# Kernel optimization log

Hardware: AMD Instinct MI355X
Metric: run time of the kernel (lower is better)

Reference implementation:

```python
import jax, jax.numpy as jnp
import numpy as np

N_NODES = 50000
N_EDGES = 800000
D = 128
N_REL = 4
N_GRAPHS = 128
N_CLASSES = 16


def rgcn_layer(x, W_rel, W_root, b, src, dst, edge_type):
    # Per-relation transform of all nodes: [N, R, D]
    xt = jnp.einsum('nd,rdf->nrf', x, W_rel)
    msg = xt[src, edge_type]  # [E, D] gather message per edge
    # mean aggregation per (dst, relation) pair (PyG RGCNConv aggr='mean')
    seg = dst * N_REL + edge_type
    cnt = jax.ops.segment_sum(jnp.ones((src.shape[0],), x.dtype), seg,
                              num_segments=N_NODES * N_REL)
    norm = 1.0 / jnp.maximum(cnt[seg], 1.0)
    agg = jax.ops.segment_sum(msg * norm[:, None], dst, num_segments=N_NODES)
    return agg + x @ W_root + b


def setup_inputs() -> dict:
    key = jax.random.key(0)
    ks = jax.random.split(key, 12)
    s = 1.0 / np.sqrt(D)
    inp = {
        'x': jax.random.normal(ks[0], (N_NODES, D), jnp.float32),
        'edge_index': jax.random.randint(ks[1], (2, N_EDGES), 0, N_NODES, jnp.int64),
        'edge_type': jax.random.randint(ks[2], (N_EDGES,), 0, N_REL, jnp.int64),
        'batch': jnp.sort(jax.random.randint(ks[3], (N_NODES,), 0, N_GRAPHS, jnp.int64)),
        'W_rel1': jax.random.normal(ks[4], (N_REL, D, D), jnp.float32) * s,
        'W_root1': jax.random.normal(ks[5], (D, D), jnp.float32) * s,
        'b1': jnp.zeros((D,), jnp.float32),
        'W_rel2': jax.random.normal(ks[6], (N_REL, D, D), jnp.float32) * s,
        'W_root2': jax.random.normal(ks[7], (D, D), jnp.float32) * s,
        'b2': jnp.zeros((D,), jnp.float32),
        'W_cls': jax.random.normal(ks[8], (D, N_CLASSES), jnp.float32) * s,
        'b_cls': jnp.zeros((N_CLASSES,), jnp.float32),
    }
    return inp


def reference(x, edge_index, edge_type, batch, W_rel1, W_root1, b1,
              W_rel2, W_root2, b2, W_cls, b_cls):
    src, dst = edge_index[0], edge_index[1]
    h = jax.nn.relu(rgcn_layer(x, W_rel1, W_root1, b1, src, dst, edge_type))
    h = jax.nn.relu(rgcn_layer(h, W_rel2, W_root2, b2, src, dst, edge_type))
    # global mean pool over graphs (dropout is identity: training=False)
    gsum = jax.ops.segment_sum(h, batch, num_segments=N_GRAPHS)
    gcnt = jax.ops.segment_sum(jnp.ones((h.shape[0],), h.dtype), batch,
                               num_segments=N_GRAPHS)
    g = gsum / jnp.maximum(gcnt, 1.0)[:, None]
    return g @ W_cls + b_cls
```

## Files before the change

kernel.cpp:

```cpp
#include <hip/hip_runtime.h>

#define D_DIM 128
#define N_REL 4
#define CAP 32

typedef __attribute__((ext_vector_type(8))) short bf16x8;
typedef __attribute__((ext_vector_type(4))) float f32x4;

static inline int cdiv(int a, int b) { return (a + b - 1) / b; }

__device__ inline ushort f2bf(float f) {
    union { float f; unsigned u; } v;
    v.f = f;
    unsigned r = v.u + 0x7FFFu + ((v.u >> 16) & 1u);
    return (ushort)(r >> 16);
}

__device__ inline float bf2f(ushort u) {
    union { unsigned u; float f; } v;
    v.u = (unsigned)u << 16;
    return v.f;
}

__device__ inline float uif(unsigned u) {
    union { unsigned u; float f; } v;
    v.u = u;
    return v.f;
}

#define CNT_B 391
#define CAST_B 6250
#define PACK_B 80

__global__ __launch_bounds__(256) void prep_kernel(
    const float* __restrict__ x, ushort* __restrict__ Xb,
    const int* __restrict__ src, const int* __restrict__ dst,
    const int* __restrict__ et, unsigned* __restrict__ icnt,
    int* __restrict__ esorted,
    const float* __restrict__ Wrel1, const float* __restrict__ Wroot1,
    const float* __restrict__ Wrel2, const float* __restrict__ Wroot2,
    ushort* __restrict__ Wpk1, ushort* __restrict__ Wpk2,
    int n4, int nEdges) {
    int b = blockIdx.x;
    if (b < CNT_B) {
        int e = (b * 256 + threadIdx.x) * 8;
        if (e >= nEdges) return;
        if (e + 8 <= nEdges) {
            int4 sA = *(const int4*)(src + e);
            int4 sB = *(const int4*)(src + e + 4);
            int4 dA = *(const int4*)(dst + e);
            int4 dB = *(const int4*)(dst + e + 4);
            int4 tA = *(const int4*)(et + e);
            int4 tB = *(const int4*)(et + e + 4);
            unsigned o0 = atomicAdd(&icnt[dA.x], 1u << (8 * tA.x));
            unsigned o1 = atomicAdd(&icnt[dA.y], 1u << (8 * tA.y));
            unsigned o2 = atomicAdd(&icnt[dA.z], 1u << (8 * tA.z));
            unsigned o3 = atomicAdd(&icnt[dA.w], 1u << (8 * tA.w));
            unsigned o4 = atomicAdd(&icnt[dB.x], 1u << (8 * tB.x));
            unsigned o5 = atomicAdd(&icnt[dB.y], 1u << (8 * tB.y));
            unsigned o6 = atomicAdd(&icnt[dB.z], 1u << (8 * tB.z));
            unsigned o7 = atomicAdd(&icnt[dB.w], 1u << (8 * tB.w));
            int r0 = (int)(((o0 >> (8 * tA.x)) & 0xFFu) - 0xAAu);
            int r1 = (int)(((o1 >> (8 * tA.y)) & 0xFFu) - 0xAAu);
            int r2 = (int)(((o2 >> (8 * tA.z)) & 0xFFu) - 0xAAu);
            int r3 = (int)(((o3 >> (8 * tA.w)) & 0xFFu) - 0xAAu);
            int r4 = (int)(((o4 >> (8 * tB.x)) & 0xFFu) - 0xAAu);
            int r5 = (int)(((o5 >> (8 * tB.y)) & 0xFFu) - 0xAAu);
            int r6 = (int)(((o6 >> (8 * tB.z)) & 0xFFu) - 0xAAu);
            int r7 = (int)(((o7 >> (8 * tB.w)) & 0xFFu) - 0xAAu);
            esorted[((size_t)(dA.x * N_REL + tA.x) << 5) + r0] = sA.x;
            esorted[((size_t)(dA.y * N_REL + tA.y) << 5) + r1] = sA.y;
            esorted[((size_t)(dA.z * N_REL + tA.z) << 5) + r2] = sA.z;
            esorted[((size_t)(dA.w * N_REL + tA.w) << 5) + r3] = sA.w;
            esorted[((size_t)(dB.x * N_REL + tB.x) << 5) + r4] = sB.x;
            esorted[((size_t)(dB.y * N_REL + tB.y) << 5) + r5] = sB.y;
            esorted[((size_t)(dB.z * N_REL + tB.z) << 5) + r6] = sB.z;
            esorted[((size_t)(dB.w * N_REL + tB.w) << 5) + r7] = sB.w;
        } else {
            for (int j = 0; e + j < nEdges; ++j) {
                int dd = dst[e + j], tt = et[e + j];
                unsigned o = atomicAdd(&icnt[dd], 1u << (8 * tt));
                int r = (int)(((o >> (8 * tt)) & 0xFFu) - 0xAAu);
                esorted[((size_t)(dd * N_REL + tt) << 5) + r] = src[e + j];
            }
        }
    } else if (b < CNT_B + CAST_B) {
        int i = (b - CNT_B) * 256 + threadIdx.x;
        if (i < n4) {
            float4 v = ((const float4*)x)[i];
            ushort4 o;
            o.x = f2bf(v.x); o.y = f2bf(v.y); o.z = f2bf(v.z); o.w = f2bf(v.w);
            ((ushort4*)Xb)[i] = o;
        }
    } else {
        int pb = b - (CNT_B + CAST_B);
        int layer = pb / 40;
        int rem = pb % 40;
        int mat = rem >> 3;
        int blk = rem & 7;
        const float* Wrel = layer ? Wrel2 : Wrel1;
        const float* Wroot = layer ? Wroot2 : Wroot1;
        ushort* out = layer ? Wpk2 : Wpk1;
        const float* W = (mat < N_REL) ? (Wrel + (size_t)mat * D_DIM * D_DIM) : Wroot;
        int t = blk * 256 + threadIdx.x;
        int lane = t & 63;
        int tile = t >> 6;
        int kt = tile >> 3;
        int nt = tile & 7;
        int n = nt * 16 + (lane & 15);
        int kb = kt * 32 + (lane >> 4) * 8;
        ushort* o = out + (((size_t)mat * 32 + tile) * 64 + lane) * 8;
        ushort4 lo, hi;
        lo.x = f2bf(W[(kb + 0) * D_DIM + n]);
        lo.y = f2bf(W[(kb + 1) * D_DIM + n]);
        lo.z = f2bf(W[(kb + 2) * D_DIM + n]);
        lo.w = f2bf(W[(kb + 3) * D_DIM + n]);
        hi.x = f2bf(W[(kb + 4) * D_DIM + n]);
        hi.y = f2bf(W[(kb + 5) * D_DIM + n]);
        hi.z = f2bf(W[(kb + 6) * D_DIM + n]);
        hi.w = f2bf(W[(kb + 7) * D_DIM + n]);
        *(ushort4*)(o) = lo;
        *(ushort4*)(o + 4) = hi;
    }
}

__global__ __launch_bounds__(256) void layer_kernel(
    const ushort* __restrict__ Xb, const unsigned* __restrict__ icnt,
    const int* __restrict__ esorted, const ushort* __restrict__ Wpk,
    const float* __restrict__ bias, ushort* __restrict__ outb, int n_nodes) {
    __shared__ ushort Ms[16][520];
    __shared__ int ids[16][33];
    __shared__ int sids[16][33];
    const int tid = threadIdx.x;
    const int wave = tid >> 6;
    const int lane = tid & 63;
    const int ql = tid & 15;
    const int qd = tid >> 4;
    const int m = lane & 15;
    const int q = lane >> 4;
    const int r0 = blockIdx.x * 16;

    auto acc8 = [](float* a, uint4 u) {
        a[0] += uif(u.x << 16); a[1] += uif(u.x & 0xFFFF0000u);
        a[2] += uif(u.y << 16); a[3] += uif(u.y & 0xFFFF0000u);
        a[4] += uif(u.z << 16); a[5] += uif(u.z & 0xFFFF0000u);
        a[6] += uif(u.w << 16); a[7] += uif(u.w & 0xFFFF0000u);
    };

    for (int p = 0; p < 4; ++p) {
        const int segl = p * 16 + qd;
        const int row = segl >> 2;
        const int rel = segl & 3;
        const int node = r0 + row;
        int deg = 0;
        if (node < n_nodes) {
            unsigned w = icnt[node];
            deg = (int)(((w >> (rel * 8)) & 0xFFu) - 0xAAu);
        }
        uint4* mrow = (uint4*)&Ms[row][rel * 128 + ql * 8];
        const ushort* xb = Xb + ql * 8;
        const int* eb = esorted + ((size_t)((node << 2) + rel) << 5);
        if (deg == 0) {
            *mrow = make_uint4(0u, 0u, 0u, 0u);
        } else if (deg == 1) {
            *mrow = *(const uint4*)(xb + (size_t)eb[0] * D_DIM);
        } else {
            for (int j = ql; j < deg; j += 16) ids[qd][j] = eb[j];
            __threadfence_block();
#pragma unroll
            for (int base = 0; base < 2; ++base) {
                int j = base * 16 + ql;
                if (j < deg) {
                    int v = ids[qd][j];
                    int rank = 0;
                    for (int k = 0; k < deg; ++k) {
                        int w = ids[qd][k];
                        rank += (w < v || (w == v && k < j)) ? 1 : 0;
                    }
                    sids[qd][rank] = v;
                }
            }
            __threadfence_block();
            float a[8], b[8];
#pragma unroll
            for (int j = 0; j < 8; ++j) { a[j] = 0.f; b[j] = 0.f; }
            int e = 0;
            for (; e + 4 <= deg; e += 4) {
                int s0 = sids[qd][e];
                int s1 = sids[qd][e + 1];
                int s2 = sids[qd][e + 2];
                int s3 = sids[qd][e + 3];
                uint4 u0 = *(const uint4*)(xb + (size_t)s0 * D_DIM);
                uint4 u1 = *(const uint4*)(xb + (size_t)s1 * D_DIM);
                uint4 u2 = *(const uint4*)(xb + (size_t)s2 * D_DIM);
                uint4 u3 = *(const uint4*)(xb + (size_t)s3 * D_DIM);
                acc8(a, u0); acc8(b, u1); acc8(a, u2); acc8(b, u3);
            }
            if (e + 2 <= deg) {
                int s0 = sids[qd][e];
                int s1 = sids[qd][e + 1];
                uint4 u0 = *(const uint4*)(xb + (size_t)s0 * D_DIM);
                uint4 u1 = *(const uint4*)(xb + (size_t)s1 * D_DIM);
                acc8(a, u0); acc8(b, u1);
                e += 2;
            }
            if (e < deg) {
                uint4 u0 = *(const uint4*)(xb + (size_t)sids[qd][e] * D_DIM);
                acc8(a, u0);
            }
            float sc = 1.0f / (float)deg;
            uint4 o;
            o.x = (unsigned)f2bf((a[0] + b[0]) * sc) | ((unsigned)f2bf((a[1] + b[1]) * sc) << 16);
            o.y = (unsigned)f2bf((a[2] + b[2]) * sc) | ((unsigned)f2bf((a[3] + b[3]) * sc) << 16);
            o.z = (unsigned)f2bf((a[4] + b[4]) * sc) | ((unsigned)f2bf((a[5] + b[5]) * sc) << 16);
            o.w = (unsigned)f2bf((a[6] + b[6]) * sc) | ((unsigned)f2bf((a[7] + b[7]) * sc) << 16);
            *mrow = o;
        }
    }
    __syncthreads();

    f32x4 acc0 = (f32x4){0.f, 0.f, 0.f, 0.f};
    f32x4 acc1 = (f32x4){0.f, 0.f, 0.f, 0.f};
#pragma unroll
    for (int ph = 0; ph < N_REL; ++ph) {
        const ushort* Bp = Wpk + (size_t)ph * (32 * 64 * 8);
#pragma unroll
        for (int kt = 0; kt < 4; ++kt) {
            bf16x8 a = *(const bf16x8*)&Ms[m][ph * 128 + kt * 32 + q * 8];
            bf16x8 b0 = *(const bf16x8*)(Bp + ((size_t)(kt * 8 + wave * 2) * 64 + lane) * 8);
            bf16x8 b1 = *(const bf16x8*)(Bp + ((size_t)(kt * 8 + wave * 2 + 1) * 64 + lane) * 8);
            acc0 = __builtin_amdgcn_mfma_f32_16x16x32_bf16(a, b0, acc0, 0, 0, 0);
            acc1 = __builtin_amdgcn_mfma_f32_16x16x32_bf16(a, b1, acc1, 0, 0, 0);
        }
    }
    {
        const int n0 = min(r0 + m, n_nodes - 1);
        const ushort* aX = Xb + (size_t)n0 * D_DIM + q * 8;
        const ushort* Bp = Wpk + (size_t)N_REL * (32 * 64 * 8);
#pragma unroll
        for (int kt = 0; kt < 4; ++kt) {
            bf16x8 a = *(const bf16x8*)(aX + kt * 32);
            bf16x8 b0 = *(const bf16x8*)(Bp + ((size_t)(kt * 8 + wave * 2) * 64 + lane) * 8);
            bf16x8 b1 = *(const bf16x8*)(Bp + ((size_t)(kt * 8 + wave * 2 + 1) * 64 + lane) * 8);
            acc0 = __builtin_amdgcn_mfma_f32_16x16x32_bf16(a, b0, acc0, 0, 0, 0);
            acc1 = __builtin_amdgcn_mfma_f32_16x16x32_bf16(a, b1, acc1, 0, 0, 0);
        }
    }

#pragma unroll
    for (int j = 0; j < 2; ++j) {
        const f32x4 av = j ? acc1 : acc0;
        int col = (wave * 2 + j) * 16 + m;
        float bv = bias[col];
#pragma unroll
        for (int r = 0; r < 4; ++r) {
            int row = r0 + q * 4 + r;
            if (row < n_nodes)
                outb[(size_t)row * D_DIM + col] = f2bf(fmaxf(av[r] + bv, 0.0f));
        }
    }
}

__global__ __launch_bounds__(1024) void poolcls_kernel(
    const ushort* __restrict__ hb, const int* __restrict__ batch,
    const float* __restrict__ Wcls, const float* __restrict__ bcls,
    float* __restrict__ out, int n_nodes) {
    __shared__ float part[64][D_DIM + 1];
    __shared__ float mean[D_DIM];
    __shared__ float cpart[16][17];
    int g = blockIdx.x;
    int tid = threadIdx.x;
    int par = tid >> 4;
    int dg = (tid & 15) * 8;
    auto lb = [&](int val) {
        int lo = 0, hi = n_nodes;
        while (lo < hi) {
            int mid = (lo + hi) >> 1;
            if (batch[mid] < val) lo = mid + 1; else hi = mid;
        }
        return lo;
    };
    int lo = lb(g), hi = lb(g + 1);
    float a[8];
#pragma unroll
    for (int j = 0; j < 8; ++j) a[j] = 0.f;
    for (int nn = lo + par; nn < hi; nn += 64) {
        uint4 u = *(const uint4*)(hb + (size_t)nn * D_DIM + dg);
        a[0] += uif(u.x << 16); a[1] += uif(u.x & 0xFFFF0000u);
        a[2] += uif(u.y << 16); a[3] += uif(u.y & 0xFFFF0000u);
        a[4] += uif(u.z << 16); a[5] += uif(u.z & 0xFFFF0000u);
        a[6] += uif(u.w << 16); a[7] += uif(u.w & 0xFFFF0000u);
    }
#pragma unroll
    for (int j = 0; j < 8; ++j) part[par][dg + j] = a[j];
    __syncthreads();
    if (tid < D_DIM) {
        float s = 0.f;
#pragma unroll
        for (int j = 0; j < 64; ++j) s += part[j][tid];
        mean[tid] = s / fmaxf((float)(hi - lo), 1.0f);
    }
    __syncthreads();
    if (tid < 256) {
        int c = tid & 15, kc = tid >> 4;
        float s = 0.f;
#pragma unroll
        for (int j = 0; j < 8; ++j)
            s = fmaf(mean[kc * 8 + j], Wcls[(kc * 8 + j) * 16 + c], s);
        cpart[kc][c] = s;
    }
    __syncthreads();
    if (tid < 16) {
        float s = bcls[tid];
#pragma unroll
        for (int k = 0; k < 16; ++k) s += cpart[k][tid];
        out[g * 16 + tid] = s;
    }
}

extern "C" void kernel_launch(void* const* d_in, const int* in_sizes, int n_in,
                              void* d_out, int out_size, void* d_ws, size_t ws_size,
                              hipStream_t stream) {
    const float* x      = (const float*)d_in[0];
    const int*   ei     = (const int*)d_in[1];
    const int*   etype  = (const int*)d_in[2];
    const int*   batch  = (const int*)d_in[3];
    const float* Wrel1  = (const float*)d_in[4];
    const float* Wroot1 = (const float*)d_in[5];
    const float* b1     = (const float*)d_in[6];
    const float* Wrel2  = (const float*)d_in[7];
    const float* Wroot2 = (const float*)d_in[8];
    const float* b2     = (const float*)d_in[9];
    const float* Wcls   = (const float*)d_in[10];
    const float* bcls   = (const float*)d_in[11];
    float* out = (float*)d_out;

    const int N = in_sizes[0] / D_DIM;
    const int E = in_sizes[1] / 2;
    const int* src = ei;
    const int* dst = ei + E;

    ushort* Xb   = (ushort*)d_ws;
    ushort* h1b  = Xb + (size_t)N * D_DIM;
    ushort* h2b  = h1b + (size_t)N * D_DIM;
    ushort* M    = h2b + (size_t)N * D_DIM;
    ushort* Wpk1 = M + (size_t)N * N_REL * D_DIM;
    ushort* Wpk2 = Wpk1 + 81920;
    unsigned* icnt = (unsigned*)(Wpk2 + 81920);
    int* esorted = (int*)(icnt + N);

    prep_kernel<<<CNT_B + CAST_B + PACK_B, 256, 0, stream>>>(
        x, Xb, src, dst, etype, icnt, esorted, Wrel1, Wroot1, Wrel2, Wroot2,
        Wpk1, Wpk2, N * D_DIM / 4, E);

    layer_kernel<<<cdiv(N, 16), 256, 0, stream>>>(
        Xb, icnt, esorted, Wpk1, b1, h1b, N);

    layer_kernel<<<cdiv(N, 16), 256, 0, stream>>>(
        h1b, icnt, esorted, Wpk2, b2, h2b, N);

    poolcls_kernel<<<128, 1024, 0, stream>>>(h2b, batch, Wcls, bcls, out, N);
}
```

Measured before the change: 270.0 us.

## Sort edge lists once in separate kernel, 16-bit ids, 32-row layer tiles

Moves the per-segment sort of source ids out of both layer kernels into a separate sort_kernel that runs once, so the two layers no longer repeat it. Edge source ids are stored as 16-bit values to halve index traffic, and each thread prefetches its id rows and counts up front. The layer kernel now handles 32 nodes per block with 512 threads, with each wave sharing one B fragment across two row tiles, and the gather loop is unrolled to 8 loads. Storing ids as ushort assumes node ids stay below 65536, which holds for 50000 nodes but not in general, and the extra kernel launch adds overhead.

```diff
diff --git a/kernel.cpp b/kernel.cpp
--- a/kernel.cpp
+++ b/kernel.cpp
@@ -36,7 +36,7 @@
     const float* __restrict__ x, ushort* __restrict__ Xb,
     const int* __restrict__ src, const int* __restrict__ dst,
     const int* __restrict__ et, unsigned* __restrict__ icnt,
-    int* __restrict__ esorted,
+    ushort* __restrict__ esorted,
     const float* __restrict__ Wrel1, const float* __restrict__ Wroot1,
     const float* __restrict__ Wrel2, const float* __restrict__ Wroot2,
     ushort* __restrict__ Wpk1, ushort* __restrict__ Wpk2,
@@ -68,20 +68,20 @@
             int r5 = (int)(((o5 >> (8 * tB.y)) & 0xFFu) - 0xAAu);
             int r6 = (int)(((o6 >> (8 * tB.z)) & 0xFFu) - 0xAAu);
             int r7 = (int)(((o7 >> (8 * tB.w)) & 0xFFu) - 0xAAu);
-            esorted[((size_t)(dA.x * N_REL + tA.x) << 5) + r0] = sA.x;
-            esorted[((size_t)(dA.y * N_REL + tA.y) << 5) + r1] = sA.y;
-            esorted[((size_t)(dA.z * N_REL + tA.z) << 5) + r2] = sA.z;
-            esorted[((size_t)(dA.w * N_REL + tA.w) << 5) + r3] = sA.w;
-            esorted[((size_t)(dB.x * N_REL + tB.x) << 5) + r4] = sB.x;
-            esorted[((size_t)(dB.y * N_REL + tB.y) << 5) + r5] = sB.y;
-            esorted[((size_t)(dB.z * N_REL + tB.z) << 5) + r6] = sB.z;
-            esorted[((size_t)(dB.w * N_REL + tB.w) << 5) + r7] = sB.w;
+            esorted[((size_t)(dA.x * N_REL + tA.x) << 5) + r0] = (ushort)sA.x;
+            esorted[((size_t)(dA.y * N_REL + tA.y) << 5) + r1] = (ushort)sA.y;
+            esorted[((size_t)(dA.z * N_REL + tA.z) << 5) + r2] = (ushort)sA.z;
+            esorted[((size_t)(dA.w * N_REL + tA.w) << 5) + r3] = (ushort)sA.w;
+            esorted[((size_t)(dB.x * N_REL + tB.x) << 5) + r4] = (ushort)sB.x;
+            esorted[((size_t)(dB.y * N_REL + tB.y) << 5) + r5] = (ushort)sB.y;
+            esorted[((size_t)(dB.z * N_REL + tB.z) << 5) + r6] = (ushort)sB.z;
+            esorted[((size_t)(dB.w * N_REL + tB.w) << 5) + r7] = (ushort)sB.w;
         } else {
             for (int j = 0; e + j < nEdges; ++j) {
                 int dd = dst[e + j], tt = et[e + j];
                 unsigned o = atomicAdd(&icnt[dd], 1u << (8 * tt));
                 int r = (int)(((o >> (8 * tt)) & 0xFFu) - 0xAAu);
-                esorted[((size_t)(dd * N_REL + tt) << 5) + r] = src[e + j];
+                esorted[((size_t)(dd * N_REL + tt) << 5) + r] = (ushort)src[e + j];
             }
         }
     } else if (b < CNT_B + CAST_B) {
@@ -124,13 +124,55 @@
     }
 }
 
-__global__ __launch_bounds__(256) void layer_kernel(
+__global__ __launch_bounds__(256) void sort_kernel(
+    const unsigned* __restrict__ icnt, ushort* __restrict__ esorted, int nseg) {
+    __shared__ int ids[16][34];
+    __shared__ int sids[16][34];
+    const int tid = threadIdx.x;
+    const int ql = tid & 15;
+    const int qd = tid >> 4;
+    const int seg = blockIdx.x * 16 + qd;
+    if (seg >= nseg) return;
+    unsigned w = icnt[seg >> 2];
+    int deg = (int)(((w >> ((seg & 3) * 8)) & 0xFFu) - 0xAAu);
+    if (deg < 2) return;
+    ushort* row = esorted + ((size_t)seg << 5);
+    unsigned u = ((const unsigned*)row)[ql];
+    ids[qd][2 * ql] = (int)(u & 0xFFFFu);
+    ids[qd][2 * ql + 1] = (int)(u >> 16);
+    __threadfence_block();
+#pragma unroll
+    for (int base = 0; base < 2; ++base) {
+        int j = base * 16 + ql;
+        if (j < deg) {
+            int v = ids[qd][j];
+            int rank = 0;
+            int k = 0;
+            for (; k + 4 <= deg; k += 4) {
+                int w0 = ids[qd][k], w1 = ids[qd][k + 1];
+                int w2 = ids[qd][k + 2], w3 = ids[qd][k + 3];
+                rank += (w0 < v || (w0 == v && k < j)) ? 1 : 0;
+                rank += (w1 < v || (w1 == v && k + 1 < j)) ? 1 : 0;
+                rank += (w2 < v || (w2 == v && k + 2 < j)) ? 1 : 0;
+                rank += (w3 < v || (w3 == v && k + 3 < j)) ? 1 : 0;
+            }
+            for (; k < deg; ++k) {
+                int wv = ids[qd][k];
+                rank += (wv < v || (wv == v && k < j)) ? 1 : 0;
+            }
+            sids[qd][rank] = v;
+        }
+    }
+    __threadfence_block();
+    for (int j = ql; j < deg; j += 16) row[j] = (ushort)sids[qd][j];
+}
+
+__global__ __launch_bounds__(512) void layer_kernel(
     const ushort* __restrict__ Xb, const unsigned* __restrict__ icnt,
-    const int* __restrict__ esorted, const ushort* __restrict__ Wpk,
+    const ushort* __restrict__ esorted, const ushort* __restrict__ Wpk,
     const float* __restrict__ bias, ushort* __restrict__ outb, int n_nodes) {
-    __shared__ ushort Ms[16][520];
-    __shared__ int ids[16][33];
-    __shared__ int sids[16][33];
+    __shared__ ushort Ms[32][520];
+    __shared__ int ids[32][34];
     const int tid = threadIdx.x;
     const int wave = tid >> 6;
     const int lane = tid & 63;
@@ -138,7 +180,20 @@
     const int qd = tid >> 4;
     const int m = lane & 15;
     const int q = lane >> 4;
-    const int r0 = blockIdx.x * 16;
+    const int r0 = blockIdx.x * 32;
+    const int rel = qd & 3;
+    const int rbase = qd >> 2;
+
+    unsigned id4[4], cnt4[4];
+#pragma unroll
+    for (int p = 0; p < 4; ++p) {
+        int node = r0 + p * 8 + rbase;
+        int vnode = min(node, n_nodes - 1);
+        cnt4[p] = icnt[vnode];
+        const ushort* eb = esorted + ((size_t)((vnode << 2) + rel) << 5);
+        id4[p] = ((const unsigned*)eb)[ql];
+        if (node >= n_nodes) cnt4[p] = 0xAAAAAAAAu;
+    }
 
     auto acc8 = [](float* a, uint4 u) {
         a[0] += uif(u.x << 16); a[1] += uif(u.x & 0xFFFF0000u);
@@ -148,74 +203,65 @@
     };
 
     for (int p = 0; p < 4; ++p) {
-        const int segl = p * 16 + qd;
-        const int row = segl >> 2;
-        const int rel = segl & 3;
-        const int node = r0 + row;
-        int deg = 0;
-        if (node < n_nodes) {
-            unsigned w = icnt[node];
-            deg = (int)(((w >> (rel * 8)) & 0xFFu) - 0xAAu);
-        }
+        const int row = p * 8 + rbase;
+        const int deg = (int)(((cnt4[p] >> (rel * 8)) & 0xFFu) - 0xAAu);
         uint4* mrow = (uint4*)&Ms[row][rel * 128 + ql * 8];
         const ushort* xb = Xb + ql * 8;
-        const int* eb = esorted + ((size_t)((node << 2) + rel) << 5);
-        if (deg == 0) {
+        if (deg <= 0) {
             *mrow = make_uint4(0u, 0u, 0u, 0u);
-        } else if (deg == 1) {
-            *mrow = *(const uint4*)(xb + (size_t)eb[0] * D_DIM);
-        } else {
-            for (int j = ql; j < deg; j += 16) ids[qd][j] = eb[j];
-            __threadfence_block();
-#pragma unroll
-            for (int base = 0; base < 2; ++base) {
-                int j = base * 16 + ql;
-                if (j < deg) {
-                    int v = ids[qd][j];
-                    int rank = 0;
-                    for (int k = 0; k < deg; ++k) {
-                        int w = ids[qd][k];
-                        rank += (w < v || (w == v && k < j)) ? 1 : 0;
-                    }
-                    sids[qd][rank] = v;
-                }
-            }
-            __threadfence_block();
-            float a[8], b[8];
-#pragma unroll
-            for (int j = 0; j < 8; ++j) { a[j] = 0.f; b[j] = 0.f; }
-            int e = 0;
-            for (; e + 4 <= deg; e += 4) {
-                int s0 = sids[qd][e];
-                int s1 = sids[qd][e + 1];
-                int s2 = sids[qd][e + 2];
-                int s3 = sids[qd][e + 3];
-                uint4 u0 = *(const uint4*)(xb + (size_t)s0 * D_DIM);
-                uint4 u1 = *(const uint4*)(xb + (size_t)s1 * D_DIM);
-                uint4 u2 = *(const uint4*)(xb + (size_t)s2 * D_DIM);
-                uint4 u3 = *(const uint4*)(xb + (size_t)s3 * D_DIM);
-                acc8(a, u0); acc8(b, u1); acc8(a, u2); acc8(b, u3);
-            }
-            if (e + 2 <= deg) {
-                int s0 = sids[qd][e];
-                int s1 = sids[qd][e + 1];
-                uint4 u0 = *(const uint4*)(xb + (size_t)s0 * D_DIM);
-                uint4 u1 = *(const uint4*)(xb + (size_t)s1 * D_DIM);
-                acc8(a, u0); acc8(b, u1);
-                e += 2;
-            }
-            if (e < deg) {
-                uint4 u0 = *(const uint4*)(xb + (size_t)sids[qd][e] * D_DIM);
-                acc8(a, u0);
-            }
-            float sc = 1.0f / (float)deg;
-            uint4 o;
-            o.x = (unsigned)f2bf((a[0] + b[0]) * sc) | ((unsigned)f2bf((a[1] + b[1]) * sc) << 16);
-            o.y = (unsigned)f2bf((a[2] + b[2]) * sc) | ((unsigned)f2bf((a[3] + b[3]) * sc) << 16);
-            o.z = (unsigned)f2bf((a[4] + b[4]) * sc) | ((unsigned)f2bf((a[5] + b[5]) * sc) << 16);
-            o.w = (unsigned)f2bf((a[6] + b[6]) * sc) | ((unsigned)f2bf((a[7] + b[7]) * sc) << 16);
-            *mrow = o;
-        }
+            continue;
+        }
+        ids[qd][2 * ql] = (int)(id4[p] & 0xFFFFu);
+        ids[qd][2 * ql + 1] = (int)(id4[p] >> 16);
+        __threadfence_block();
+        float a[8], b[8];
+#pragma unroll
+        for (int j = 0; j < 8; ++j) { a[j] = 0.f; b[j] = 0.f; }
+        int e = 0;
+        for (; e + 8 <= deg; e += 8) {
+            int s0 = ids[qd][e],     s1 = ids[qd][e + 1];
+            int s2 = ids[qd][e + 2], s3 = ids[qd][e + 3];
+            int s4 = ids[qd][e + 4], s5 = ids[qd][e + 5];
+            int s6 = ids[qd][e + 6], s7 = ids[qd][e + 7];
+            uint4 u0 = *(const uint4*)(xb + (size_t)s0 * D_DIM);
+            uint4 u1 = *(const uint4*)(xb + (size_t)s1 * D_DIM);
+            uint4 u2 = *(const uint4*)(xb + (size_t)s2 * D_DIM);
+            uint4 u3 = *(const uint4*)(xb + (size_t)s3 * D_DIM);
+            uint4 u4 = *(const uint4*)(xb + (size_t)s4 * D_DIM);
+            uint4 u5 = *(const uint4*)(xb + (size_t)s5 * D_DIM);
+            uint4 u6 = *(const uint4*)(xb + (size_t)s6 * D_DIM);
+            uint4 u7 = *(const uint4*)(xb + (size_t)s7 * D_DIM);
+            acc8(a, u0); acc8(b, u1); acc8(a, u2); acc8(b, u3);
+            acc8(a, u4); acc8(b, u5); acc8(a, u6); acc8(b, u7);
+        }
+        if (e + 4 <= deg) {
+            int s0 = ids[qd][e], s1 = ids[qd][e + 1];
+            int s2 = ids[qd][e + 2], s3 = ids[qd][e + 3];
+            uint4 u0 = *(const uint4*)(xb + (size_t)s0 * D_DIM);
+            uint4 u1 = *(const uint4*)(xb + (size_t)s1 * D_DIM);
+            uint4 u2 = *(const uint4*)(xb + (size_t)s2 * D_DIM);
+            uint4 u3 = *(const uint4*)(xb + (size_t)s3 * D_DIM);
+            acc8(a, u0); acc8(b, u1); acc8(a, u2); acc8(b, u3);
+            e += 4;
+        }
+        if (e + 2 <= deg) {
+            int s0 = ids[qd][e], s1 = ids[qd][e + 1];
+            uint4 u0 = *(const uint4*)(xb + (size_t)s0 * D_DIM);
+            uint4 u1 = *(const uint4*)(xb + (size_t)s1 * D_DIM);
+            acc8(a, u0); acc8(b, u1);
+            e += 2;
+        }
+        if (e < deg) {
+            uint4 u0 = *(const uint4*)(xb + (size_t)ids[qd][e] * D_DIM);
+            acc8(a, u0);
+        }
+        float sc = 1.0f / (float)deg;
+        uint4 o;
+        o.x = (unsigned)f2bf((a[0] + b[0]) * sc) | ((unsigned)f2bf((a[1] + b[1]) * sc) << 16);
+        o.y = (unsigned)f2bf((a[2] + b[2]) * sc) | ((unsigned)f2bf((a[3] + b[3]) * sc) << 16);
+        o.z = (unsigned)f2bf((a[4] + b[4]) * sc) | ((unsigned)f2bf((a[5] + b[5]) * sc) << 16);
+        o.w = (unsigned)f2bf((a[6] + b[6]) * sc) | ((unsigned)f2bf((a[7] + b[7]) * sc) << 16);
+        *mrow = o;
     }
     __syncthreads();
 
@@ -223,40 +269,42 @@
     f32x4 acc1 = (f32x4){0.f, 0.f, 0.f, 0.f};
 #pragma unroll
     for (int ph = 0; ph < N_REL; ++ph) {
-        const ushort* Bp = Wpk + (size_t)ph * (32 * 64 * 8);
 #pragma unroll
         for (int kt = 0; kt < 4; ++kt) {
-            bf16x8 a = *(const bf16x8*)&Ms[m][ph * 128 + kt * 32 + q * 8];
-            bf16x8 b0 = *(const bf16x8*)(Bp + ((size_t)(kt * 8 + wave * 2) * 64 + lane) * 8);
-            bf16x8 b1 = *(const bf16x8*)(Bp + ((size_t)(kt * 8 + wave * 2 + 1) * 64 + lane) * 8);
-            acc0 = __builtin_amdgcn_mfma_f32_16x16x32_bf16(a, b0, acc0, 0, 0, 0);
-            acc1 = __builtin_amdgcn_mfma_f32_16x16x32_bf16(a, b1, acc1, 0, 0, 0);
+            bf16x8 b = *(const bf16x8*)(Wpk + (((size_t)ph * 32 + kt * 8 + wave) * 64 + lane) * 8);
+            bf16x8 a0 = *(const bf16x8*)&Ms[m][ph * 128 + kt * 32 + q * 8];
+            bf16x8 a1 = *(const bf16x8*)&Ms[16 + m][ph * 128 + kt * 32 + q * 8];
+            acc0 = __builtin_amdgcn_mfma_f32_16x16x32_bf16(a0, b, acc0, 0, 0, 0);
+            acc1 = __builtin_amdgcn_mfma_f32_16x16x32_bf16(a1, b, acc1, 0, 0, 0);
         }
     }
     {
         const int n0 = min(r0 + m, n_nodes - 1);
-        const ushort* aX = Xb + (size_t)n0 * D_DIM + q * 8;
-        const ushort* Bp = Wpk + (size_t)N_REL * (32 * 64 * 8);
+        const int n1 = min(r0 + 16 + m, n_nodes - 1);
+        const ushort* aX0 = Xb + (size_t)n0 * D_DIM + q * 8;
+        const ushort* aX1 = Xb + (size_t)n1 * D_DIM + q * 8;
 #pragma unroll
         for (int kt = 0; kt < 4; ++kt) {
-            bf16x8 a = *(const bf16x8*)(aX + kt * 32);
-            bf16x8 b0 = *(const bf16x8*)(Bp + ((size_t)(kt * 8 + wave * 2) * 64 + lane) * 8);
-            bf16x8 b1 = *(const bf16x8*)(Bp + ((size_t)(kt * 8 + wave * 2 + 1) * 64 + lane) * 8);
-            acc0 = __builtin_amdgcn_mfma_f32_16x16x32_bf16(a, b0, acc0, 0, 0, 0);
-            acc1 = __builtin_amdgcn_mfma_f32_16x16x32_bf16(a, b1, acc1, 0, 0, 0);
-        }
-    }
-
-#pragma unroll
-    for (int j = 0; j < 2; ++j) {
-        const f32x4 av = j ? acc1 : acc0;
-        int col = (wave * 2 + j) * 16 + m;
+            bf16x8 b = *(const bf16x8*)(Wpk + (((size_t)N_REL * 32 + kt * 8 + wave) * 64 + lane) * 8);
+            bf16x8 a0 = *(const bf16x8*)(aX0 + kt * 32);
+            bf16x8 a1 = *(const bf16x8*)(aX1 + kt * 32);
+            acc0 = __builtin_amdgcn_mfma_f32_16x16x32_bf16(a0, b, acc0, 0, 0, 0);
+            acc1 = __builtin_amdgcn_mfma_f32_16x16x32_bf16(a1, b, acc1, 0, 0, 0);
+        }
+    }
+
+    {
+        int col = wave * 16 + m;
         float bv = bias[col];
 #pragma unroll
-        for (int r = 0; r < 4; ++r) {
-            int row = r0 + q * 4 + r;
-            if (row < n_nodes)
-                outb[(size_t)row * D_DIM + col] = f2bf(fmaxf(av[r] + bv, 0.0f));
+        for (int rt = 0; rt < 2; ++rt) {
+            const f32x4 av = rt ? acc1 : acc0;
+#pragma unroll
+            for (int r = 0; r < 4; ++r) {
+                int row = r0 + rt * 16 + q * 4 + r;
+                if (row < n_nodes)
+                    outb[(size_t)row * D_DIM + col] = f2bf(fmaxf(av[r] + bv, 0.0f));
+            }
         }
     }
 }
@@ -337,26 +385,28 @@
 
     const int N = in_sizes[0] / D_DIM;
     const int E = in_sizes[1] / 2;
+    const int NSEG = N * N_REL;
     const int* src = ei;
     const int* dst = ei + E;
 
     ushort* Xb   = (ushort*)d_ws;
     ushort* h1b  = Xb + (size_t)N * D_DIM;
     ushort* h2b  = h1b + (size_t)N * D_DIM;
-    ushort* M    = h2b + (size_t)N * D_DIM;
-    ushort* Wpk1 = M + (size_t)N * N_REL * D_DIM;
+    ushort* Wpk1 = h2b + (size_t)N * D_DIM;
     ushort* Wpk2 = Wpk1 + 81920;
     unsigned* icnt = (unsigned*)(Wpk2 + 81920);
-    int* esorted = (int*)(icnt + N);
+    ushort* esorted = (ushort*)(icnt + N);
 
     prep_kernel<<<CNT_B + CAST_B + PACK_B, 256, 0, stream>>>(
         x, Xb, src, dst, etype, icnt, esorted, Wrel1, Wroot1, Wrel2, Wroot2,
         Wpk1, Wpk2, N * D_DIM / 4, E);
 
-    layer_kernel<<<cdiv(N, 16), 256, 0, stream>>>(
+    sort_kernel<<<cdiv(NSEG, 16), 256, 0, stream>>>(icnt, esorted, NSEG);
+
+    layer_kernel<<<cdiv(N, 32), 512, 0, stream>>>(
         Xb, icnt, esorted, Wpk1, b1, h1b, N);
 
-    layer_kernel<<<cdiv(N, 16), 256, 0, stream>>>(
+    layer_kernel<<<cdiv(N, 32), 512, 0, stream>>>(
         h1b, icnt, esorted, Wpk2, b2, h2b, N);
 
     poolcls_kernel<<<128, 1024, 0, stream>>>(h2b, batch, Wcls, bcls, out, N);
```

New measurement: 269.1 us. Within noise of the previous version (-0.3%).
